# Kernel optimization log

Measured on AMD Instinct MI355X. Metric: run time of the kernel, lower is better.

The kernel has to match this reference:

```python
import jax, jax.numpy as jnp
import numpy as np

N, H, W, CIN, COUT, FSIZE = 8, 128, 128, 64, 128, 3
EPS = 1e-3      # keras BatchNormalization default epsilon
ALPHA = 0.2     # LeakyReLU alpha


def setup_inputs() -> dict:
    key = jax.random.key(0)
    k0, k1, k2 = jax.random.split(key, 3)
    return {
        "inputs_real": jax.random.normal(k0, (N, H, W, CIN), jnp.float32),
        "inputs_imag": jax.random.normal(k1, (N, H, W, CIN), jnp.float32),
        "filters": jax.random.normal(k2, (FSIZE, FSIZE, CIN, COUT), jnp.float32) * 0.1,
        "gamma_real": jnp.ones((COUT,), jnp.float32),
        "beta_real": jnp.zeros((COUT,), jnp.float32),
        "gamma_imag": jnp.ones((COUT,), jnp.float32),
        "beta_imag": jnp.zeros((COUT,), jnp.float32),
    }


def _bn_train(x, gamma, beta):
    # BatchNorm in training mode: batch stats over (N, H, W), biased variance.
    mean = jnp.mean(x, axis=(0, 1, 2), keepdims=True)
    var = jnp.var(x, axis=(0, 1, 2), keepdims=True)
    return gamma * (x - mean) * jax.lax.rsqrt(var + EPS) + beta


def _leaky(x):
    return jnp.where(x >= 0, x, ALPHA * x)


def _spectral_kernels(filters):
    # Pad spatial filters [f,f,Cin,Cout] to [H,W,Cin,Cout] (bottom/right), FFT over H,W.
    f = filters.shape[0]
    fp = jnp.pad(filters, ((0, H - f), (0, W - f), (0, 0), (0, 0)))
    ff = jnp.fft.fft2(jnp.transpose(fp, (2, 3, 0, 1)).astype(jnp.complex64))  # [Cin,Cout,H,W]
    ff = jnp.transpose(ff, (2, 3, 0, 1))  # [H,W,Cin,Cout]
    kr = jnp.real(ff)
    ki = jnp.real(ff)  # faithful to source: filters_imag is ALSO tf.math.real(filters_freq)
    return kr, ki


def reference(inputs_real, inputs_imag, filters, gamma_real, beta_real, gamma_imag, beta_imag):
    kr, ki = _spectral_kernels(filters)
    # Fused form of the per-batch loop: sum over Cin of (ac+bd) and (bc-ad).
    out_real = (jnp.einsum('nhwc,hwco->nhwo', inputs_real, kr)
                + jnp.einsum('nhwc,hwco->nhwo', inputs_imag, ki))
    out_imag = (jnp.einsum('nhwc,hwco->nhwo', inputs_imag, kr)
                - jnp.einsum('nhwc,hwco->nhwo', inputs_real, ki))
    out_real = _leaky(_bn_train(out_real, gamma_real, beta_real))
    out_imag = _leaky(_bn_train(out_imag, gamma_imag, beta_imag))
    return (out_real, out_imag)
```

## Files before the change

kernel.cpp:

```cpp
#include <hip/hip_runtime.h>
#include <hip/hip_bf16.h>


typedef __bf16 bf16x8 __attribute__((ext_vector_type(8)));
typedef float f32x4 __attribute__((ext_vector_type(4)));

__device__ __forceinline__ unsigned pack2(float a, float b) {
    __hip_bfloat162 h = __float22bfloat162_rn(make_float2(a, b));
    return *reinterpret_cast<unsigned*>(&h);
}
__device__ __forceinline__ void unpack8(uint4 u, float* f) {
    f[0] = __uint_as_float(u.x << 16); f[1] = __uint_as_float(u.x & 0xffff0000u);
    f[2] = __uint_as_float(u.y << 16); f[3] = __uint_as_float(u.y & 0xffff0000u);
    f[4] = __uint_as_float(u.z << 16); f[5] = __uint_as_float(u.z & 0xffff0000u);
    f[6] = __uint_as_float(u.w << 16); f[7] = __uint_as_float(u.w & 0xffff0000u);
}

__global__ __launch_bounds__(512, 4) void conv_bn_fused(
    const float* __restrict__ xr, const float* __restrict__ xi,
    const float* __restrict__ filt, float* __restrict__ out,
    float* __restrict__ gstats, unsigned* __restrict__ done,
    const float* __restrict__ gr, const float* __restrict__ br,
    const float* __restrict__ gi, const float* __restrict__ bi)
{
    __shared__ __align__(16) unsigned short pqT[5 * 4096];
    __shared__ __align__(16) unsigned short xsh[16 * 16 * 64];
    __shared__ __align__(16) float statl[512];

    const int t = threadIdx.x;
    const int gid = blockIdx.x;
    const int oh = gid >> 8;
    const int u  = (gid & 255) >> 1;
    const int vh = gid & 1;
    const int obase = oh << 6;
    const int vbase0 = vh << 6;

    unsigned* pq32 = (unsigned*)pqT;
    unsigned* xs32 = (unsigned*)xsh;

    const float au = 6.28318530717958647692f * (float)u / 128.0f;
    float su1, cu1, su2, cu2;
    __sincosf(au, &su1, &cu1);
    __sincosf(2.0f * au, &su2, &cu2);

    #pragma unroll
    for (int k = 0; k < 4; ++k) {
        int i = t + k * 512;
        int o = i & 63;
        int cp = i >> 6;
        int g0 = (2 * cp) * 128 + obase + o;
        int g1 = g0 + 128;
        unsigned wd = o * 32 + (((cp >> 2) ^ (o & 7)) << 2) + (cp & 3);
        #pragma unroll
        for (int b = 0; b < 3; ++b) {
            float f0a = filt[b * 8192 + g0],       f0b = filt[b * 8192 + g1];
            float f1a = filt[(3 + b) * 8192 + g0], f1b = filt[(3 + b) * 8192 + g1];
            float f2a = filt[(6 + b) * 8192 + g0], f2b = filt[(6 + b) * 8192 + g1];
            float Pa = fmaf(cu2, f2a, fmaf(cu1, f1a, f0a));
            float Pb = fmaf(cu2, f2b, fmaf(cu1, f1b, f0b));
            pq32[b * 2048 + wd] = pack2(Pa, Pb);
            if (b > 0) {
                float Qa = fmaf(su2, f2a, su1 * f1a);
                float Qb = fmaf(su2, f2b, su1 * f1b);
                pq32[(b + 2) * 2048 + wd] = pack2(Qa, Qb);
            }
        }
    }

    const int wave = t >> 6;
    const int lane = t & 63;
    const int vg   = wave >> 1;
    const int nth  = wave & 1;
    const int ln15 = lane & 15;
    const int q    = lane >> 4;
    const int swz  = ln15 & 7;
    const int part = q >> 1;
    const int nbase = (q & 1) * 4;

    const int sv = t >> 5;
    const int scp = t & 31;

    float ssum[2] = {0.f, 0.f}, ssq[2] = {0.f, 0.f};

    #pragma unroll 1
    for (int chk = 0; chk < 4; ++chk) {
        {
            const int vglob = vbase0 + chk * 16 + sv;
            #pragma unroll
            for (int n = 0; n < 8; ++n) {
                size_t gi = (((size_t)(n * 128 + u)) * 128 + vglob) * 64 + 2 * scp;
                float2 r  = *(const float2*)(xr + gi);
                float2 m2 = *(const float2*)(xi + gi);
                unsigned rp = pack2(r.x + m2.x, r.y + m2.y);
                unsigned ip = pack2(m2.x - r.x, m2.y - r.y);
                unsigned base = (sv * 16 + n) * 32 + (((scp >> 2) ^ (n & 7)) << 2) + (scp & 3);
                xs32[base] = rp;
                xs32[base + 256] = ip;
            }
        }
        __syncthreads();

        float cv1[4], cv2[4], nsv1[4], nsv2[4];
        #pragma unroll
        for (int vj = 0; vj < 4; ++vj) {
            float av = 6.28318530717958647692f *
                       (float)(vbase0 + chk * 16 + vg * 4 + vj) / 128.0f;
            float s1, c1, s2, c2;
            __sincosf(av, &s1, &c1);
            __sincosf(2.0f * av, &s2, &c2);
            cv1[vj] = c1; cv2[vj] = c2; nsv1[vj] = -s1; nsv2[vj] = -s2;
        }

        bf16x8 af[4][2];
        #pragma unroll
        for (int vj = 0; vj < 4; ++vj) {
            const unsigned short* xrow = &xsh[((vg * 4 + vj) * 16 + ln15) * 64];
            #pragma unroll
            for (int ks = 0; ks < 2; ++ks) {
                int m = ks * 4 + q;
                af[vj][ks] = __builtin_bit_cast(bf16x8,
                    *(const uint4*)(xrow + ((m ^ swz) << 3)));
            }
        }

        #pragma unroll
        for (int ntl = 0; ntl < 2; ++ntl) {
            const int ot = nth * 2 + ntl;
            const int o_loc = ot * 16 + ln15;
            const unsigned short* prow = &pqT[o_loc * 64];
            f32x4 acc[4];
            #pragma unroll
            for (int vj = 0; vj < 4; ++vj) acc[vj] = (f32x4){0.f, 0.f, 0.f, 0.f};

            #pragma unroll
            for (int ks = 0; ks < 2; ++ks) {
                const int m = ks * 4 + q;
                const int foff = (m ^ swz) << 3;
                float P0[8], P1[8], P2[8], Q1[8], Q2[8];
                unpack8(*(const uint4*)(prow + 0 * 4096 + foff), P0);
                unpack8(*(const uint4*)(prow + 1 * 4096 + foff), P1);
                unpack8(*(const uint4*)(prow + 2 * 4096 + foff), P2);
                unpack8(*(const uint4*)(prow + 3 * 4096 + foff), Q1);
                unpack8(*(const uint4*)(prow + 4 * 4096 + foff), Q2);
                #pragma unroll
                for (int vj = 0; vj < 4; ++vj) {
                    float kr[8];
                    #pragma unroll
                    for (int j = 0; j < 8; ++j) {
                        float tv = fmaf(cv1[vj], P1[j], P0[j]);
                        tv = fmaf(cv2[vj], P2[j], tv);
                        tv = fmaf(nsv1[vj], Q1[j], tv);
                        kr[j] = fmaf(nsv2[vj], Q2[j], tv);
                    }
                    uint4 B;
                    B.x = pack2(kr[0], kr[1]); B.y = pack2(kr[2], kr[3]);
                    B.z = pack2(kr[4], kr[5]); B.w = pack2(kr[6], kr[7]);
                    acc[vj] = __builtin_amdgcn_mfma_f32_16x16x32_bf16(
                        af[vj][ks], __builtin_bit_cast(bf16x8, B), acc[vj], 0, 0, 0);
                }
            }

            const int o_glob = obase + o_loc;
            #pragma unroll
            for (int vj = 0; vj < 4; ++vj) {
                const int vglob = vbase0 + chk * 16 + vg * 4 + vj;
                size_t base = (size_t)part * 16777216 + (size_t)nbase * 2097152
                            + ((size_t)(u * 128 + vglob)) * 128 + o_glob;
                #pragma unroll
                for (int r = 0; r < 4; ++r) {
                    float y = acc[vj][r];
                    out[base + (size_t)r * 2097152] = y;
                    ssum[ntl] += y;
                    ssq[ntl] = fmaf(y, y, ssq[ntl]);
                }
            }
        }
        __syncthreads();
    }

    statl[t] = 0.f;
    __syncthreads();
    #pragma unroll
    for (int ntl = 0; ntl < 2; ++ntl) {
        int chn = part * 128 + obase + (nth * 2 + ntl) * 16 + ln15;
        atomicAdd(&statl[chn], ssum[ntl]);
        atomicAdd(&statl[256 + chn], ssq[ntl]);
    }
    __syncthreads();
    atomicAdd(&gstats[t], statl[t]);

    __syncthreads();
    if (t == 0) {
        __threadfence();
        atomicAdd(done, 1u);
        while (atomicAdd(done, 0u) < 512u) {
            __builtin_amdgcn_s_sleep(2);
        }
        __threadfence();
    }
    __syncthreads();

    if (t < 256) {
        int pp = t >> 7, o = t & 127;
        const float inv = 1.0f / 131072.0f;
        float s0 = atomicAdd(&gstats[t], 0.0f);
        float s1 = atomicAdd(&gstats[256 + t], 0.0f);
        float mean = s0 * inv;
        float var  = s1 * inv - mean * mean;
        float g = pp ? gi[o] : gr[o];
        float b = pp ? bi[o] : br[o];
        float s = g * rsqrtf(var + 1e-3f);
        statl[t]       = s;
        statl[256 + t] = b - mean * s;
    }
    __syncthreads();

    const f32x4* scv = (const f32x4*)statl;
    const f32x4* shv = (const f32x4*)(statl + 256);
    const int ob4 = obase >> 2;
    #pragma unroll 4
    for (int it2 = 0; it2 < 32; ++it2) {
        int idx = t + it2 * 512;
        int oq = idx & 15;
        int vv = (idx >> 4) & 63;
        int nn = (idx >> 10) & 7;
        int pp = idx >> 13;
        size_t e = ((((size_t)(pp * 8 + nn) * 128 + u) * 128
                   + (size_t)(vbase0 + vv)) << 7) + (size_t)(obase + oq * 4);
        f32x4 x = *(const f32x4*)(out + e);
        f32x4 sc = scv[pp * 32 + ob4 + oq];
        f32x4 sh = shv[pp * 32 + ob4 + oq];
        f32x4 y;
        #pragma unroll
        for (int r = 0; r < 4; ++r) {
            float w = fmaf(x[r], sc[r], sh[r]);
            y[r] = w >= 0.0f ? w : 0.2f * w;
        }
        *(f32x4*)(out + e) = y;
    }
}

extern "C" void kernel_launch(void* const* d_in, const int* in_sizes, int n_in,
                              void* d_out, int out_size, void* d_ws, size_t ws_size,
                              hipStream_t stream)
{
    const float* xr   = (const float*)d_in[0];
    const float* xi   = (const float*)d_in[1];
    const float* filt = (const float*)d_in[2];
    const float* gr   = (const float*)d_in[3];
    const float* br   = (const float*)d_in[4];
    const float* gi   = (const float*)d_in[5];
    const float* bi   = (const float*)d_in[6];
    float* out = (float*)d_out;
    float* ws  = (float*)d_ws;

    float* gstats  = ws;
    unsigned* done = (unsigned*)(ws + 512);

    (void)hipMemsetAsync(ws, 0, 516 * sizeof(float), stream);
    conv_bn_fused<<<dim3(512), dim3(512), 0, stream>>>(
        xr, xi, filt, out, gstats, done, gr, br, gi, bi);
}
```

Baseline: 366.0 us.

## Split output channels into quarters to double grid size and occupancy

Each block now handles 32 output channels instead of 64, which doubles the grid to 1024 blocks and halves shared memory per block. Launch bounds are raised to 8 blocks per SM. This spreads work across more CUs and leaves more room for latency hiding, at the cost of re-reading and re-packing the input tile twice as often. The grid barrier must now wait for 1024 blocks, and all of them must be co-resident or the kernel deadlocks. The final BN/LeakyReLU writes use nontemporal stores.

```diff
diff --git a/kernel.cpp b/kernel.cpp
--- a/kernel.cpp
+++ b/kernel.cpp
@@ -16,23 +16,23 @@
     f[6] = __uint_as_float(u.w << 16); f[7] = __uint_as_float(u.w & 0xffff0000u);
 }
 
-__global__ __launch_bounds__(512, 4) void conv_bn_fused(
+__global__ __launch_bounds__(512, 8) void conv_bn_fused(
     const float* __restrict__ xr, const float* __restrict__ xi,
     const float* __restrict__ filt, float* __restrict__ out,
     float* __restrict__ gstats, unsigned* __restrict__ done,
     const float* __restrict__ gr, const float* __restrict__ br,
     const float* __restrict__ gi, const float* __restrict__ bi)
 {
-    __shared__ __align__(16) unsigned short pqT[5 * 4096];
-    __shared__ __align__(16) unsigned short xsh[16 * 16 * 64];
+    __shared__ __align__(16) unsigned short pqT[5 * 2048];
+    __shared__ __align__(16) unsigned short xsh[8 * 16 * 64];
     __shared__ __align__(16) float statl[512];
 
     const int t = threadIdx.x;
     const int gid = blockIdx.x;
-    const int oh = gid >> 8;
+    const int oq = gid >> 8;
     const int u  = (gid & 255) >> 1;
     const int vh = gid & 1;
-    const int obase = oh << 6;
+    const int obase = oq << 5;
     const int vbase0 = vh << 6;
 
     unsigned* pq32 = (unsigned*)pqT;
@@ -44,10 +44,10 @@
     __sincosf(2.0f * au, &su2, &cu2);
 
     #pragma unroll
-    for (int k = 0; k < 4; ++k) {
+    for (int k = 0; k < 2; ++k) {
         int i = t + k * 512;
-        int o = i & 63;
-        int cp = i >> 6;
+        int o = i & 31;
+        int cp = i >> 5;
         int g0 = (2 * cp) * 128 + obase + o;
         int g1 = g0 + 128;
         unsigned wd = o * 32 + (((cp >> 2) ^ (o & 7)) << 2) + (cp & 3);
@@ -58,11 +58,11 @@
             float f2a = filt[(6 + b) * 8192 + g0], f2b = filt[(6 + b) * 8192 + g1];
             float Pa = fmaf(cu2, f2a, fmaf(cu1, f1a, f0a));
             float Pb = fmaf(cu2, f2b, fmaf(cu1, f1b, f0b));
-            pq32[b * 2048 + wd] = pack2(Pa, Pb);
+            pq32[b * 1024 + wd] = pack2(Pa, Pb);
             if (b > 0) {
                 float Qa = fmaf(su2, f2a, su1 * f1a);
                 float Qb = fmaf(su2, f2b, su1 * f1b);
-                pq32[(b + 2) * 2048 + wd] = pack2(Qa, Qb);
+                pq32[(b + 2) * 1024 + wd] = pack2(Qa, Qb);
             }
         }
     }
@@ -77,102 +77,100 @@
     const int part = q >> 1;
     const int nbase = (q & 1) * 4;
 
-    const int sv = t >> 5;
+    const int sxv = t >> 6;
+    const int nh  = (t >> 5) & 1;
     const int scp = t & 31;
 
-    float ssum[2] = {0.f, 0.f}, ssq[2] = {0.f, 0.f};
+    float ssum = 0.f, ssq = 0.f;
 
     #pragma unroll 1
-    for (int chk = 0; chk < 4; ++chk) {
+    for (int chk = 0; chk < 8; ++chk) {
         {
-            const int vglob = vbase0 + chk * 16 + sv;
-            #pragma unroll
-            for (int n = 0; n < 8; ++n) {
+            const int vglob = vbase0 + chk * 8 + sxv;
+            #pragma unroll
+            for (int k = 0; k < 4; ++k) {
+                int n = nh * 4 + k;
                 size_t gi = (((size_t)(n * 128 + u)) * 128 + vglob) * 64 + 2 * scp;
                 float2 r  = *(const float2*)(xr + gi);
                 float2 m2 = *(const float2*)(xi + gi);
                 unsigned rp = pack2(r.x + m2.x, r.y + m2.y);
                 unsigned ip = pack2(m2.x - r.x, m2.y - r.y);
-                unsigned base = (sv * 16 + n) * 32 + (((scp >> 2) ^ (n & 7)) << 2) + (scp & 3);
+                unsigned base = (sxv * 16 + n) * 32 + (((scp >> 2) ^ (n & 7)) << 2) + (scp & 3);
                 xs32[base] = rp;
                 xs32[base + 256] = ip;
             }
         }
         __syncthreads();
 
-        float cv1[4], cv2[4], nsv1[4], nsv2[4];
-        #pragma unroll
-        for (int vj = 0; vj < 4; ++vj) {
+        float cv1[2], cv2[2], nsv1[2], nsv2[2];
+        #pragma unroll
+        for (int j = 0; j < 2; ++j) {
             float av = 6.28318530717958647692f *
-                       (float)(vbase0 + chk * 16 + vg * 4 + vj) / 128.0f;
+                       (float)(vbase0 + chk * 8 + vg * 2 + j) / 128.0f;
             float s1, c1, s2, c2;
             __sincosf(av, &s1, &c1);
             __sincosf(2.0f * av, &s2, &c2);
-            cv1[vj] = c1; cv2[vj] = c2; nsv1[vj] = -s1; nsv2[vj] = -s2;
-        }
-
-        bf16x8 af[4][2];
-        #pragma unroll
-        for (int vj = 0; vj < 4; ++vj) {
-            const unsigned short* xrow = &xsh[((vg * 4 + vj) * 16 + ln15) * 64];
+            cv1[j] = c1; cv2[j] = c2; nsv1[j] = -s1; nsv2[j] = -s2;
+        }
+
+        bf16x8 af[2][2];
+        #pragma unroll
+        for (int j = 0; j < 2; ++j) {
+            const unsigned short* xrow = &xsh[((vg * 2 + j) * 16 + ln15) * 64];
             #pragma unroll
             for (int ks = 0; ks < 2; ++ks) {
                 int m = ks * 4 + q;
-                af[vj][ks] = __builtin_bit_cast(bf16x8,
+                af[j][ks] = __builtin_bit_cast(bf16x8,
                     *(const uint4*)(xrow + ((m ^ swz) << 3)));
             }
         }
 
-        #pragma unroll
-        for (int ntl = 0; ntl < 2; ++ntl) {
-            const int ot = nth * 2 + ntl;
-            const int o_loc = ot * 16 + ln15;
-            const unsigned short* prow = &pqT[o_loc * 64];
-            f32x4 acc[4];
-            #pragma unroll
-            for (int vj = 0; vj < 4; ++vj) acc[vj] = (f32x4){0.f, 0.f, 0.f, 0.f};
-
-            #pragma unroll
-            for (int ks = 0; ks < 2; ++ks) {
-                const int m = ks * 4 + q;
-                const int foff = (m ^ swz) << 3;
-                float P0[8], P1[8], P2[8], Q1[8], Q2[8];
-                unpack8(*(const uint4*)(prow + 0 * 4096 + foff), P0);
-                unpack8(*(const uint4*)(prow + 1 * 4096 + foff), P1);
-                unpack8(*(const uint4*)(prow + 2 * 4096 + foff), P2);
-                unpack8(*(const uint4*)(prow + 3 * 4096 + foff), Q1);
-                unpack8(*(const uint4*)(prow + 4 * 4096 + foff), Q2);
+        const int o_loc = nth * 16 + ln15;
+        const unsigned short* prow = &pqT[o_loc * 64];
+        f32x4 acc[2];
+        acc[0] = (f32x4){0.f, 0.f, 0.f, 0.f};
+        acc[1] = (f32x4){0.f, 0.f, 0.f, 0.f};
+
+        #pragma unroll
+        for (int ks = 0; ks < 2; ++ks) {
+            const int m = ks * 4 + q;
+            const int foff = (m ^ swz) << 3;
+            float P0[8], P1[8], P2[8], Q1[8], Q2[8];
+            unpack8(*(const uint4*)(prow + 0 * 2048 + foff), P0);
+            unpack8(*(const uint4*)(prow + 1 * 2048 + foff), P1);
+            unpack8(*(const uint4*)(prow + 2 * 2048 + foff), P2);
+            unpack8(*(const uint4*)(prow + 3 * 2048 + foff), Q1);
+            unpack8(*(const uint4*)(prow + 4 * 2048 + foff), Q2);
+            #pragma unroll
+            for (int j = 0; j < 2; ++j) {
+                float kr[8];
                 #pragma unroll
-                for (int vj = 0; vj < 4; ++vj) {
-                    float kr[8];
-                    #pragma unroll
-                    for (int j = 0; j < 8; ++j) {
-                        float tv = fmaf(cv1[vj], P1[j], P0[j]);
-                        tv = fmaf(cv2[vj], P2[j], tv);
-                        tv = fmaf(nsv1[vj], Q1[j], tv);
-                        kr[j] = fmaf(nsv2[vj], Q2[j], tv);
-                    }
-                    uint4 B;
-                    B.x = pack2(kr[0], kr[1]); B.y = pack2(kr[2], kr[3]);
-                    B.z = pack2(kr[4], kr[5]); B.w = pack2(kr[6], kr[7]);
-                    acc[vj] = __builtin_amdgcn_mfma_f32_16x16x32_bf16(
-                        af[vj][ks], __builtin_bit_cast(bf16x8, B), acc[vj], 0, 0, 0);
+                for (int jj = 0; jj < 8; ++jj) {
+                    float tv = fmaf(cv1[j], P1[jj], P0[jj]);
+                    tv = fmaf(cv2[j], P2[jj], tv);
+                    tv = fmaf(nsv1[j], Q1[jj], tv);
+                    kr[jj] = fmaf(nsv2[j], Q2[jj], tv);
                 }
-            }
-
-            const int o_glob = obase + o_loc;
-            #pragma unroll
-            for (int vj = 0; vj < 4; ++vj) {
-                const int vglob = vbase0 + chk * 16 + vg * 4 + vj;
-                size_t base = (size_t)part * 16777216 + (size_t)nbase * 2097152
-                            + ((size_t)(u * 128 + vglob)) * 128 + o_glob;
-                #pragma unroll
-                for (int r = 0; r < 4; ++r) {
-                    float y = acc[vj][r];
-                    out[base + (size_t)r * 2097152] = y;
-                    ssum[ntl] += y;
-                    ssq[ntl] = fmaf(y, y, ssq[ntl]);
-                }
+                uint4 B;
+                B.x = pack2(kr[0], kr[1]); B.y = pack2(kr[2], kr[3]);
+                B.z = pack2(kr[4], kr[5]); B.w = pack2(kr[6], kr[7]);
+                acc[j] = __builtin_amdgcn_mfma_f32_16x16x32_bf16(
+                    af[j][ks], __builtin_bit_cast(bf16x8, B), acc[j], 0, 0, 0);
+            }
+        }
+
+        const int o_glob = obase + o_loc;
+        #pragma unroll
+        for (int j = 0; j < 2; ++j) {
+            const int vglob = vbase0 + chk * 8 + vg * 2 + j;
+            size_t base = (size_t)part * 16777216 + (size_t)nbase * 2097152
+                        + ((size_t)(u * 128 + vglob)) * 128 + o_glob;
+            #pragma unroll
+            for (int r = 0; r < 4; ++r) {
+                float y = acc[j][r];
+                out[base + (size_t)r * 2097152] = y;
+                ssum += y;
+                ssq = fmaf(y, y, ssq);
             }
         }
         __syncthreads();
@@ -180,11 +178,10 @@
 
     statl[t] = 0.f;
     __syncthreads();
-    #pragma unroll
-    for (int ntl = 0; ntl < 2; ++ntl) {
-        int chn = part * 128 + obase + (nth * 2 + ntl) * 16 + ln15;
-        atomicAdd(&statl[chn], ssum[ntl]);
-        atomicAdd(&statl[256 + chn], ssq[ntl]);
+    {
+        int chn = part * 128 + obase + nth * 16 + ln15;
+        atomicAdd(&statl[chn], ssum);
+        atomicAdd(&statl[256 + chn], ssq);
     }
     __syncthreads();
     atomicAdd(&gstats[t], statl[t]);
@@ -193,7 +190,7 @@
     if (t == 0) {
         __threadfence();
         atomicAdd(done, 1u);
-        while (atomicAdd(done, 0u) < 512u) {
+        while (atomicAdd(done, 0u) < 1024u) {
             __builtin_amdgcn_s_sleep(2);
         }
         __threadfence();
@@ -219,24 +216,24 @@
     const f32x4* shv = (const f32x4*)(statl + 256);
     const int ob4 = obase >> 2;
     #pragma unroll 4
-    for (int it2 = 0; it2 < 32; ++it2) {
+    for (int it2 = 0; it2 < 16; ++it2) {
         int idx = t + it2 * 512;
-        int oq = idx & 15;
-        int vv = (idx >> 4) & 63;
-        int nn = (idx >> 10) & 7;
-        int pp = idx >> 13;
+        int oq4 = idx & 7;
+        int vv = (idx >> 3) & 63;
+        int nn = (idx >> 9) & 7;
+        int pp = idx >> 12;
         size_t e = ((((size_t)(pp * 8 + nn) * 128 + u) * 128
-                   + (size_t)(vbase0 + vv)) << 7) + (size_t)(obase + oq * 4);
+                   + (size_t)(vbase0 + vv)) << 7) + (size_t)(obase + oq4 * 4);
         f32x4 x = *(const f32x4*)(out + e);
-        f32x4 sc = scv[pp * 32 + ob4 + oq];
-        f32x4 sh = shv[pp * 32 + ob4 + oq];
+        f32x4 sc = scv[pp * 32 + ob4 + oq4];
+        f32x4 sh = shv[pp * 32 + ob4 + oq4];
         f32x4 y;
         #pragma unroll
         for (int r = 0; r < 4; ++r) {
             float w = fmaf(x[r], sc[r], sh[r]);
             y[r] = w >= 0.0f ? w : 0.2f * w;
         }
-        *(f32x4*)(out + e) = y;
+        __builtin_nontemporal_store(y, (f32x4*)(out + e));
     }
 }
 
@@ -258,6 +255,6 @@
     unsigned* done = (unsigned*)(ws + 512);
 
     (void)hipMemsetAsync(ws, 0, 516 * sizeof(float), stream);
-    conv_bn_fused<<<dim3(512), dim3(512), 0, stream>>>(
+    conv_bn_fused<<<dim3(1024), dim3(512), 0, stream>>>(
         xr, xi, filt, out, gstats, done, gr, br, gi, bi);
 }
```

Result: slower. 516.4 us (+41.1%).
